# Kernel tuning notes

Hardware: AMD Instinct MI355X
Metric: run time of the kernel (lower is better)

Reference implementation:

```python
import jax, jax.numpy as jnp
import numpy as np

N_NODES = 100000


def setup_inputs() -> dict:
    key = jax.random.key(0)
    k1, k2, k3 = jax.random.split(key, 3)
    feat = jax.random.normal(k1, (N_NODES, 64), dtype=jnp.float32)
    src = jax.random.randint(k2, (1250000,), 0, N_NODES, dtype=jnp.int64)
    dst = jax.random.randint(k3, (1250000,), 0, N_NODES, dtype=jnp.int64)
    return {"feat": feat, "src": src, "dst": dst}


def reference(feat, src, dst):
    # GraphConv(norm='both', activation=None): degree-normalized neighbor sum
    # with implicit self-connection (rst = feat_dst + sum_neighbors), where
    # degrees are clamp(min=1) + 1 to account for the self edge.
    n = feat.shape[0]
    ones = jnp.ones(src.shape[0], dtype=feat.dtype)
    out_deg = jax.ops.segment_sum(ones, src, num_segments=n)
    in_deg = jax.ops.segment_sum(ones, dst, num_segments=n)
    norm_l = jax.lax.rsqrt(jnp.maximum(out_deg, 1.0) + 1.0)  # [N]
    norm_r = jax.lax.rsqrt(jnp.maximum(in_deg, 1.0) + 1.0)   # [N]
    feat_src = feat * norm_l[:, None]                         # left-normalize
    msgs = feat_src[src]                                      # gather [E, D]
    h_neigh = jax.ops.segment_sum(msgs, dst, num_segments=n)  # scatter-sum [N, D]
    rst = (feat + h_neigh) * norm_r[:, None]                  # right-normalize
    return rst
```

## Files before the change

### kernel.cpp

```cpp
#include <hip/hip_runtime.h>


#define GC_D 64
#define PSIZE 196
#define SCAP 3072
#define EPB 8192
#define MAXPART 512
#define GC_CAP 64


__global__ __launch_bounds__(512) void partition_kernel(
        const int* __restrict__ src,
        const int* __restrict__ dst,
        int* __restrict__ curA,
        int* __restrict__ curB,
        int* __restrict__ streamA,
        unsigned char* __restrict__ streamB,
        int e, int nPart) {
    __shared__ int histA[MAXPART], histB[MAXPART], baseA[MAXPART], baseB[MAXPART];
    __shared__ int lcurA[MAXPART], lcurB[MAXPART];
    int t = threadIdx.x;
    for (int i = t; i < nPart; i += 512) {
        histA[i] = 0; histB[i] = 0; lcurA[i] = 0; lcurB[i] = 0;
    }
    __syncthreads();
    int lo = blockIdx.x * EPB;
    int hi = min(lo + EPB, e);
    for (int i = lo + t; i < hi; i += 512) {
        int s = src[i], d = dst[i];
        atomicAdd(&histA[d / PSIZE], 1);
        atomicAdd(&histB[s / PSIZE], 1);
    }
    __syncthreads();
    for (int i = t; i < nPart; i += 512) {
        int hA = histA[i];
        baseA[i] = hA ? atomicAdd(&curA[i], hA) : 0;
        int hB = histB[i];
        baseB[i] = hB ? atomicAdd(&curB[i], hB) : 0;
    }
    __syncthreads();
    for (int i = lo + t; i < hi; i += 512) {
        int s = src[i], d = dst[i];
        int pA = d / PSIZE;
        int posA = baseA[pA] + atomicAdd(&lcurA[pA], 1);
        if (posA < SCAP) streamA[pA * SCAP + posA] = s | ((d - pA * PSIZE) << 17);
        int pB = s / PSIZE;
        int posB = baseB[pB] + atomicAdd(&lcurB[pB], 1);
        if (posB < SCAP) streamB[pB * SCAP + posB] = (unsigned char)(s - pB * PSIZE);
    }
}

__global__ __launch_bounds__(512) void convertB_kernel(
        const int* __restrict__ curB,
        const unsigned char* __restrict__ streamB,
        const float* __restrict__ feat,
        unsigned short* __restrict__ featb,
        int n) {
    __shared__ int lodeg[256];
    int p = blockIdx.x, t = threadIdx.x;
    if (t < 256) lodeg[t] = 0;
    __syncthreads();
    int cB = min(curB[p], SCAP);
    const unsigned char* sB = streamB + (size_t)p * SCAP;
    for (int i = t; i < cB; i += 512) atomicAdd(&lodeg[sB[i]], 1);
    __syncthreads();
    int wave = t >> 6, lane = t & 63;
    int g = p * PSIZE;
    for (int r = wave; r < PSIZE; r += 8) {
        int node = g + r;
        if (node >= n) break;
        float nl = rsqrtf(fmaxf((float)lodeg[r], 1.0f) + 1.0f);
        float v = feat[(size_t)node * GC_D + lane] * nl;
        unsigned bb = __float_as_uint(v);
        bb = (bb + 0x7FFFu + ((bb >> 16) & 1u)) >> 16;
        featb[(size_t)node * GC_D + lane] = (unsigned short)bb;
    }
    if (p == 0 && t < GC_D) featb[(size_t)n * GC_D + t] = 0;
}

__global__ __launch_bounds__(1024) void sortgather_kernel(
        const int* __restrict__ curA,
        const int* __restrict__ streamA,
        const float* __restrict__ feat,
        const unsigned short* __restrict__ featb,
        float* __restrict__ out,
        int n) {
    __shared__ int sAl[SCAP];
    __shared__ int lperm[SCAP];
    __shared__ int lcnt[256], loff[256], lcur[256];
    int p = blockIdx.x, t = threadIdx.x;
    if (t < 256) lcnt[t] = 0;
    __syncthreads();
    int cA = min(curA[p], SCAP);
    const int* sA = streamA + (size_t)p * SCAP;
    for (int i = t; i < cA; i += 1024) {
        int v = sA[i];
        sAl[i] = v;
        atomicAdd(&lcnt[(v >> 17) & 255], 1);
    }
    __syncthreads();
    if (t < 256) loff[t] = lcnt[t];
    __syncthreads();
    for (int off = 1; off < 256; off <<= 1) {
        int a = (t < 256 && t >= off) ? loff[t - off] : 0;
        __syncthreads();
        if (t < 256) loff[t] += a;
        __syncthreads();
    }
    if (t < 256) { loff[t] -= lcnt[t]; lcur[t] = 0; }
    __syncthreads();
    for (int i = t; i < cA; i += 1024) {
        int v = sAl[i];
        int bin = (v >> 17) & 255;
        int pos = loff[bin] + atomicAdd(&lcur[bin], 1);
        lperm[pos] = v & 0x1FFFF;
    }
    __syncthreads();
    int wave = t >> 6, lane = t & 63;
    int half = lane >> 5;
    int c = lane & 31;
    int g = p * PSIZE;
    for (int r = wave; r < PSIZE; r += 16) {
        int node = g + r;
        if (node >= n) break;
        int deg = lcnt[r];
        int off = loff[r];
        float acc0 = 0.0f, acc1 = 0.0f;
        for (int base = 0; base < deg; base += 64) {
            int m = min(deg - base, 64);
            int s_l = (lane < m) ? lperm[off + base + lane] : n;
            int m16 = (m + 15) & ~15;
            for (int j = 0; j < m16; j += 16) {
#pragma unroll
                for (int k = 0; k < 8; ++k) {
                    int s = __shfl(s_l, j + 2 * k + half);
                    unsigned u = *(const unsigned*)(featb + (size_t)s * GC_D + 2 * c);
                    acc0 += __uint_as_float(u << 16);
                    acc1 += __uint_as_float(u & 0xFFFF0000u);
                }
            }
        }
        acc0 += __shfl_xor(acc0, 32);
        acc1 += __shfl_xor(acc1, 32);
        if (half == 0) {
            float nr = rsqrtf(fmaxf((float)deg, 1.0f) + 1.0f);
            const float2 self = *(const float2*)(feat + (size_t)node * GC_D + 2 * c);
            float2 rr;
            rr.x = (self.x + acc0) * nr;
            rr.y = (self.y + acc1) * nr;
            *(float2*)(out + (size_t)node * GC_D + 2 * c) = rr;
        }
    }
}


__global__ void zero_int_kernel(int* __restrict__ p, int n) {
    int i = blockIdx.x * blockDim.x + threadIdx.x;
    if (i < n) p[i] = 0;
}

__global__ void bucket_hist_kernel(const int* __restrict__ src,
                                   const int* __restrict__ dst,
                                   int* __restrict__ cnt,
                                   int* __restrict__ outdeg,
                                   int* __restrict__ bucket,
                                   int e) {
    int i = blockIdx.x * blockDim.x + threadIdx.x;
    if (i < e) {
        int s = src[i];
        int d = dst[i];
        atomicAdd(&outdeg[s], 1);
        int pos = atomicAdd(&cnt[d], 1);
        if (pos < GC_CAP) bucket[d * GC_CAP + pos] = s;
    }
}

__global__ void convert_kernel(const float* __restrict__ feat,
                               const int* __restrict__ outdeg,
                               unsigned short* __restrict__ featb,
                               int n) {
    int i = blockIdx.x * blockDim.x + threadIdx.x;
    int total = (n + 1) * GC_D;
    if (i >= total) return;
    int row = i >> 6;
    if (row >= n) { featb[i] = 0; return; }
    float nl = rsqrtf(fmaxf((float)outdeg[row], 1.0f) + 1.0f);
    unsigned b = __float_as_uint(feat[i] * nl);
    b = (b + 0x7FFFu + ((b >> 16) & 1u)) >> 16;
    featb[i] = (unsigned short)b;
}

__global__ __launch_bounds__(256) void gather_bf16_kernel(
        const float* __restrict__ feat,
        const unsigned short* __restrict__ featb,
        const int* __restrict__ bucket,
        const int* __restrict__ cnt,
        float* __restrict__ out,
        int n) {
    int wid = (blockIdx.x * blockDim.x + threadIdx.x) >> 6;
    int lane = threadIdx.x & 63;
    if (wid >= n) return;
    int deg = cnt[wid];
    int s_raw = bucket[wid * GC_CAP + lane];
    int m = min(deg, GC_CAP);
    int s_l = (lane < m) ? s_raw : n;
    int half = lane >> 5;
    int c = lane & 31;
    float acc0 = 0.0f, acc1 = 0.0f;
    int m16 = (m + 15) & ~15;
    for (int j = 0; j < m16; j += 16) {
#pragma unroll
        for (int k = 0; k < 8; ++k) {
            int s = __shfl(s_l, j + 2 * k + half);
            unsigned u = *(const unsigned*)(featb + (size_t)s * GC_D + 2 * c);
            acc0 += __uint_as_float(u << 16);
            acc1 += __uint_as_float(u & 0xFFFF0000u);
        }
    }
    acc0 += __shfl_xor(acc0, 32);
    acc1 += __shfl_xor(acc1, 32);
    if (half == 0) {
        float nr = rsqrtf(fmaxf((float)deg, 1.0f) + 1.0f);
        const float2 self = *(const float2*)(feat + (size_t)wid * GC_D + 2 * c);
        float2 r;
        r.x = (self.x + acc0) * nr;
        r.y = (self.y + acc1) * nr;
        *(float2*)(out + (size_t)wid * GC_D + 2 * c) = r;
    }
}


extern "C" void kernel_launch(void* const* d_in, const int* in_sizes, int n_in,
                              void* d_out, int out_size, void* d_ws, size_t ws_size,
                              hipStream_t stream) {
    const float* feat = (const float*)d_in[0];
    const int*   src  = (const int*)d_in[1];
    const int*   dst  = (const int*)d_in[2];
    float* out = (float*)d_out;

    const int n = in_sizes[0] / GC_D;
    const int e = in_sizes[1];
    const int nPart = (n + PSIZE - 1) / PSIZE;

    size_t featb_ints = ((size_t)(n + 1) * GC_D + 1) / 2;
    size_t o = 2 * (size_t)nPart;
    o = (o + 31) & ~(size_t)31;
    size_t streamA_o = o;  o += (size_t)nPart * SCAP;
    size_t featb_o = o;    o += featb_ints;
    size_t need_main = o * sizeof(int) + (size_t)nPart * SCAP;

    size_t featb_bytes = (size_t)(n + 1) * GC_D * sizeof(unsigned short);
    size_t need_bf16 = ((size_t)2 * n + (size_t)n * GC_CAP) * sizeof(int) + featb_bytes;

    bool main_ok = (ws_size >= need_main) && nPart <= MAXPART && n <= 131071;

    if (main_ok) {
        int* ws = (int*)d_ws;
        int* curA = ws;
        int* curB = ws + nPart;
        int* streamA = ws + streamA_o;
        unsigned short* featb = (unsigned short*)(ws + featb_o);
        unsigned char* streamB = (unsigned char*)(ws + o);

        hipMemsetAsync(curA, 0, 2 * (size_t)nPart * sizeof(int), stream);
        partition_kernel<<<(e + EPB - 1) / EPB, 512, 0, stream>>>(
            src, dst, curA, curB, streamA, streamB, e, nPart);
        convertB_kernel<<<nPart, 512, 0, stream>>>(curB, streamB, feat, featb, n);
        sortgather_kernel<<<nPart, 1024, 0, stream>>>(curA, streamA, feat, featb,
                                                      out, n);
    } else if (ws_size >= need_bf16) {
        int* cnt    = (int*)d_ws;
        int* outdeg = cnt + n;
        int* bucket = outdeg + n;
        unsigned short* featb = (unsigned short*)(bucket + (size_t)n * GC_CAP);

        zero_int_kernel<<<(2 * n + 255) / 256, 256, 0, stream>>>(cnt, 2 * n);
        bucket_hist_kernel<<<(e + 255) / 256, 256, 0, stream>>>(src, dst, cnt,
                                                                outdeg, bucket, e);
        int totalc = (n + 1) * GC_D;
        convert_kernel<<<(totalc + 255) / 256, 256, 0, stream>>>(feat, outdeg,
                                                                 featb, n);
        long long total = (long long)n * GC_D;
        gather_bf16_kernel<<<(int)((total + 255) / 256), 256, 0, stream>>>(
            feat, featb, bucket, cnt, out, n);
    }
}
```

Before: 154.8 us.

## Split partition into separate dst/src block jobs and widen bf16 gather loads

The partition kernel now launches twice as many blocks, each handling either the dst-keyed stream or the src-keyed stream. This halves per-block shared memory and per-thread work and gives more parallelism for the atomic-heavy binning (153 blocks become 306). Each wave in the gather kernel now covers four neighbors per step with 8-byte bf16 loads across 16 lanes, instead of two neighbors with 4-byte loads. That issues fewer, wider loads but needs an extra shuffle-reduction stage and rereads src/dst across the two block groups.

```diff
diff --git a/kernel.cpp b/kernel.cpp
--- a/kernel.cpp
+++ b/kernel.cpp
@@ -16,37 +16,39 @@
         int* __restrict__ curB,
         int* __restrict__ streamA,
         unsigned char* __restrict__ streamB,
-        int e, int nPart) {
-    __shared__ int histA[MAXPART], histB[MAXPART], baseA[MAXPART], baseB[MAXPART];
-    __shared__ int lcurA[MAXPART], lcurB[MAXPART];
+        int e, int nPart, int nBlkE) {
+    __shared__ int hist[MAXPART], base[MAXPART], lcur[MAXPART];
     int t = threadIdx.x;
+    bool jobA = blockIdx.x < nBlkE;
+    int b = jobA ? blockIdx.x : blockIdx.x - nBlkE;
+    for (int i = t; i < nPart; i += 512) { hist[i] = 0; lcur[i] = 0; }
+    __syncthreads();
+    int lo = b * EPB;
+    int hi = min(lo + EPB, e);
+    const int* key = jobA ? dst : src;
+    for (int i = lo + t; i < hi; i += 512)
+        atomicAdd(&hist[key[i] / PSIZE], 1);
+    __syncthreads();
+    int* cur = jobA ? curA : curB;
     for (int i = t; i < nPart; i += 512) {
-        histA[i] = 0; histB[i] = 0; lcurA[i] = 0; lcurB[i] = 0;
-    }
-    __syncthreads();
-    int lo = blockIdx.x * EPB;
-    int hi = min(lo + EPB, e);
-    for (int i = lo + t; i < hi; i += 512) {
-        int s = src[i], d = dst[i];
-        atomicAdd(&histA[d / PSIZE], 1);
-        atomicAdd(&histB[s / PSIZE], 1);
-    }
-    __syncthreads();
-    for (int i = t; i < nPart; i += 512) {
-        int hA = histA[i];
-        baseA[i] = hA ? atomicAdd(&curA[i], hA) : 0;
-        int hB = histB[i];
-        baseB[i] = hB ? atomicAdd(&curB[i], hB) : 0;
-    }
-    __syncthreads();
-    for (int i = lo + t; i < hi; i += 512) {
-        int s = src[i], d = dst[i];
-        int pA = d / PSIZE;
-        int posA = baseA[pA] + atomicAdd(&lcurA[pA], 1);
-        if (posA < SCAP) streamA[pA * SCAP + posA] = s | ((d - pA * PSIZE) << 17);
-        int pB = s / PSIZE;
-        int posB = baseB[pB] + atomicAdd(&lcurB[pB], 1);
-        if (posB < SCAP) streamB[pB * SCAP + posB] = (unsigned char)(s - pB * PSIZE);
+        int h = hist[i];
+        base[i] = h ? atomicAdd(&cur[i], h) : 0;
+    }
+    __syncthreads();
+    if (jobA) {
+        for (int i = lo + t; i < hi; i += 512) {
+            int d = dst[i];
+            int pA = d / PSIZE;
+            int pos = base[pA] + atomicAdd(&lcur[pA], 1);
+            if (pos < SCAP) streamA[pA * SCAP + pos] = src[i] | ((d - pA * PSIZE) << 17);
+        }
+    } else {
+        for (int i = lo + t; i < hi; i += 512) {
+            int s = src[i];
+            int pB = s / PSIZE;
+            int pos = base[pB] + atomicAdd(&lcur[pB], 1);
+            if (pos < SCAP) streamB[pB * SCAP + pos] = (unsigned char)(s - pB * PSIZE);
+        }
     }
 }
 
@@ -117,38 +119,48 @@
     }
     __syncthreads();
     int wave = t >> 6, lane = t & 63;
-    int half = lane >> 5;
-    int c = lane & 31;
+    int q = lane >> 4;
+    int c = lane & 15;
     int g = p * PSIZE;
     for (int r = wave; r < PSIZE; r += 16) {
         int node = g + r;
         if (node >= n) break;
         int deg = lcnt[r];
         int off = loff[r];
-        float acc0 = 0.0f, acc1 = 0.0f;
+        float a0 = 0.f, a1 = 0.f, a2 = 0.f, a3 = 0.f;
         for (int base = 0; base < deg; base += 64) {
             int m = min(deg - base, 64);
             int s_l = (lane < m) ? lperm[off + base + lane] : n;
             int m16 = (m + 15) & ~15;
             for (int j = 0; j < m16; j += 16) {
+                uint2 u[4];
 #pragma unroll
-                for (int k = 0; k < 8; ++k) {
-                    int s = __shfl(s_l, j + 2 * k + half);
-                    unsigned u = *(const unsigned*)(featb + (size_t)s * GC_D + 2 * c);
-                    acc0 += __uint_as_float(u << 16);
-                    acc1 += __uint_as_float(u & 0xFFFF0000u);
+                for (int k = 0; k < 4; ++k) {
+                    int s = __shfl(s_l, j + 4 * k + q);
+                    u[k] = *(const uint2*)(featb + (size_t)s * GC_D + 4 * c);
+                }
+#pragma unroll
+                for (int k = 0; k < 4; ++k) {
+                    a0 += __uint_as_float(u[k].x << 16);
+                    a1 += __uint_as_float(u[k].x & 0xFFFF0000u);
+                    a2 += __uint_as_float(u[k].y << 16);
+                    a3 += __uint_as_float(u[k].y & 0xFFFF0000u);
                 }
             }
         }
-        acc0 += __shfl_xor(acc0, 32);
-        acc1 += __shfl_xor(acc1, 32);
-        if (half == 0) {
+        a0 += __shfl_xor(a0, 16); a0 += __shfl_xor(a0, 32);
+        a1 += __shfl_xor(a1, 16); a1 += __shfl_xor(a1, 32);
+        a2 += __shfl_xor(a2, 16); a2 += __shfl_xor(a2, 32);
+        a3 += __shfl_xor(a3, 16); a3 += __shfl_xor(a3, 32);
+        if (q == 0) {
             float nr = rsqrtf(fmaxf((float)deg, 1.0f) + 1.0f);
-            const float2 self = *(const float2*)(feat + (size_t)node * GC_D + 2 * c);
-            float2 rr;
-            rr.x = (self.x + acc0) * nr;
-            rr.y = (self.y + acc1) * nr;
-            *(float2*)(out + (size_t)node * GC_D + 2 * c) = rr;
+            const float4 self = *(const float4*)(feat + (size_t)node * GC_D + 4 * c);
+            float4 rr;
+            rr.x = (self.x + a0) * nr;
+            rr.y = (self.y + a1) * nr;
+            rr.z = (self.z + a2) * nr;
+            rr.w = (self.w + a3) * nr;
+            *(float4*)(out + (size_t)node * GC_D + 4 * c) = rr;
         }
     }
 }
@@ -241,6 +253,7 @@
     const int n = in_sizes[0] / GC_D;
     const int e = in_sizes[1];
     const int nPart = (n + PSIZE - 1) / PSIZE;
+    const int nBlkE = (e + EPB - 1) / EPB;
 
     size_t featb_ints = ((size_t)(n + 1) * GC_D + 1) / 2;
     size_t o = 2 * (size_t)nPart;
@@ -263,8 +276,8 @@
         unsigned char* streamB = (unsigned char*)(ws + o);
 
         hipMemsetAsync(curA, 0, 2 * (size_t)nPart * sizeof(int), stream);
-        partition_kernel<<<(e + EPB - 1) / EPB, 512, 0, stream>>>(
-            src, dst, curA, curB, streamA, streamB, e, nPart);
+        partition_kernel<<<2 * nBlkE, 512, 0, stream>>>(
+            src, dst, curA, curB, streamA, streamB, e, nPart, nBlkE);
         convertB_kernel<<<nPart, 512, 0, stream>>>(curB, streamB, feat, featb, n);
         sortgather_kernel<<<nPart, 1024, 0, stream>>>(curA, streamA, feat, featb,
                                                       out, n);
```

Measured after the change: 157.4 us. About the same (+1.7%).
